# Kernel tuning notes

Hardware: AMD Instinct MI355X
Metric: run time of the kernel (lower is better)

## Reference

```python
import jax, jax.numpy as jnp
import numpy as np

B, S, E, H = 2, 2048, 1024, 16
D = E // H  # head dim = 64
ROPE_BASE = 10000.0


def _rope(x):
    # x: [B, H, S, D]; interleaved-pair rotary embeddings (torchtune style)
    d2 = D // 2
    theta = 1.0 / (ROPE_BASE ** (jnp.arange(d2, dtype=jnp.float32) * 2.0 / D))  # [D/2]
    pos = jnp.arange(S, dtype=jnp.float32)
    ang = pos[:, None] * theta[None, :]            # [S, D/2]
    cos, sin = jnp.cos(ang), jnp.sin(ang)          # broadcast over B,H
    xr = x.reshape(B, H, S, d2, 2)
    x1, x2 = xr[..., 0], xr[..., 1]
    o1 = x1 * cos - x2 * sin
    o2 = x1 * sin + x2 * cos
    return jnp.stack([o1, o2], axis=-1).reshape(B, H, S, D)


def setup_inputs() -> dict:
    key = jax.random.key(0)
    ks = jax.random.split(key, 5)
    scale = 1.0 / np.sqrt(E)
    return {
        "x": jax.random.normal(ks[0], (B, S, E), dtype=jnp.float32),
        "Wq": jax.random.normal(ks[1], (E, E), dtype=jnp.float32) * scale,
        "Wk": jax.random.normal(ks[2], (E, E), dtype=jnp.float32) * scale,
        "Wv": jax.random.normal(ks[3], (E, E), dtype=jnp.float32) * scale,
        "Wo": jax.random.normal(ks[4], (E, E), dtype=jnp.float32) * scale,
    }


def reference(x, Wq, Wk, Wv, Wo):
    # torch Linear: y = x @ W^T
    def proj(W):
        return (x @ W.T).reshape(B, S, H, D).transpose(0, 2, 1, 3)  # [B,H,S,D]

    q = _rope(proj(Wq))
    k = _rope(proj(Wk))
    v = proj(Wv)

    attn_scale = 1.0 / np.sqrt(E)  # faithful: scales by sqrt(d_embed), not head dim
    scores = jnp.einsum('bhqd,bhkd->bhqk', q, k) * attn_scale  # [B,H,S,S]
    causal = jnp.tril(jnp.ones((S, S), dtype=bool))
    scores = jnp.where(causal, scores, -jnp.inf)
    probs = jax.nn.softmax(scores, axis=-1)
    out = jnp.einsum('bhqk,bhkd->bhqd', probs, v)  # [B,H,S,D]
    out = out.transpose(0, 2, 1, 3).reshape(B, S, E)
    return out @ Wo.T
```

## Files before the change

kernel.cpp:

```cpp
#include <hip/hip_runtime.h>
#include <hip/hip_bf16.h>
#include <math.h>

typedef __bf16 bf16;
typedef __bf16 bf16x8 __attribute__((ext_vector_type(8)));
typedef float f32x4 __attribute__((ext_vector_type(4)));

#define SEQ 2048
#define EMB 1024
#define NH  16
#define HD  64
#define NROWS 4096

#define GLOAD_LDS16(gp, lp)                                             \
    __builtin_amdgcn_global_load_lds(                                   \
        (const __attribute__((address_space(1))) void*)(gp),            \
        (__attribute__((address_space(3))) void*)(lp), 16, 0, 0)

__global__ __launch_bounds__(256) void cvt_kernel(
    const float* __restrict__ x,  const float* __restrict__ Wq,
    const float* __restrict__ Wk, const float* __restrict__ Wv,
    const float* __restrict__ Wo,
    bf16* __restrict__ xb, bf16* __restrict__ Wqb, bf16* __restrict__ Wkb,
    bf16* __restrict__ Wvb, bf16* __restrict__ Wob)
{
    int b = blockIdx.x;
    const float* src; bf16* dst; int boff;
    if      (b < 2048) { src = x;  dst = xb;  boff = b;        }
    else if (b < 2560) { src = Wq; dst = Wqb; boff = b - 2048; }
    else if (b < 3072) { src = Wk; dst = Wkb; boff = b - 2560; }
    else if (b < 3584) { src = Wv; dst = Wvb; boff = b - 3072; }
    else               { src = Wo; dst = Wob; boff = b - 3584; }
    size_t off = (size_t)boff * 2048 + (size_t)threadIdx.x * 8;
    float4 f0 = *(const float4*)(src + off);
    float4 f1 = *(const float4*)(src + off + 4);
    bf16x8 v;
    v[0] = (bf16)f0.x; v[1] = (bf16)f0.y; v[2] = (bf16)f0.z; v[3] = (bf16)f0.w;
    v[4] = (bf16)f1.x; v[5] = (bf16)f1.y; v[6] = (bf16)f1.z; v[7] = (bf16)f1.w;
    *(bf16x8*)(dst + off) = v;
}

__global__ void rope_table_kernel(float* __restrict__ ctab, float* __restrict__ stab) {
    int t = blockIdx.x * blockDim.x + threadIdx.x;
    int s = t >> 5;
    int j = t & 31;
    double freq = pow(10000.0, -(double)j / 32.0);
    double ang = (double)s * freq;
    ctab[t] = (float)cos(ang);
    stab[t] = (float)sin(ang);
}

__global__ __launch_bounds__(256) void qkv_rope_kernel(
    const bf16* __restrict__ x,
    const bf16* __restrict__ Wq, const bf16* __restrict__ Wk, const bf16* __restrict__ Wv,
    const float* __restrict__ ctab, const float* __restrict__ stab,
    bf16* __restrict__ q_ws, bf16* __restrict__ kf_ws, bf16* __restrict__ vf_ws)
{
    __shared__ __align__(16) bf16 As[128 * 32];
    __shared__ __align__(16) bf16 Bs[128 * 32];

    const int t    = threadIdx.x;
    const int lane = t & 63;
    const int wave = t >> 6;
    const int col  = lane & 15;
    const int quad = lane >> 4;

    const int nblk = blockIdx.x;
    const int m0   = blockIdx.y * 128;

    const bf16* W; int nloc;
    if (nblk < 8)       { W = Wq; nloc = nblk * 128; }
    else if (nblk < 16) { W = Wk; nloc = (nblk - 8) * 128; }
    else                { W = Wv; nloc = (nblk - 16) * 128; }

    const bf16 *ga[2], *gb[2];
#pragma unroll
    for (int j = 0; j < 2; j++) {
        int c = t + j * 256;
        ga[j] = x + (size_t)(m0 + (c >> 2)) * EMB + (c & 3) * 8;
        gb[j] = W + (size_t)(nloc + (c >> 2)) * EMB + (c & 3) * 8;
    }

    const int wm = (wave >> 1) * 64;
    const int wn = (wave & 1) * 64;

    f32x4 acc[4][4];
#pragma unroll
    for (int i = 0; i < 4; i++)
#pragma unroll
        for (int j = 0; j < 4; j++) acc[i][j] = (f32x4){0.f, 0.f, 0.f, 0.f};

    for (int kc = 0; kc < EMB; kc += 32) {
#pragma unroll
        for (int j = 0; j < 2; j++) {
            int c = t + j * 256;
            GLOAD_LDS16(ga[j] + kc, As + c * 8);
            GLOAD_LDS16(gb[j] + kc, Bs + c * 8);
        }
        __syncthreads();
        bf16x8 a[4], b[4];
#pragma unroll
        for (int mt = 0; mt < 4; mt++)
            a[mt] = *(const bf16x8*)(As + (wm + mt * 16 + col) * 32 + quad * 8);
#pragma unroll
        for (int nt = 0; nt < 4; nt++)
            b[nt] = *(const bf16x8*)(Bs + (wn + nt * 16 + col) * 32 + quad * 8);
#pragma unroll
        for (int mt = 0; mt < 4; mt++)
#pragma unroll
            for (int nt = 0; nt < 4; nt++)
                acc[mt][nt] = __builtin_amdgcn_mfma_f32_16x16x32_bf16(a[mt], b[nt], acc[mt][nt], 0, 0, 0);
        __syncthreads();
    }

    const int n0w = nblk * 128 + wn;
    const int m0w = m0 + wm;
#pragma unroll
    for (int mt = 0; mt < 4; mt++) {
#pragma unroll
        for (int nt = 0; nt < 4; nt++) {
            int n  = n0w + nt * 16 + col;
            int d  = n & 63;
            int h  = (n >> 6) & 15;
            int jj = d >> 1;
#pragma unroll
            for (int r = 0; r < 4; r++) {
                int m  = m0w + mt * 16 + quad * 4 + r;
                int bb_ = m >> 11;
                int ss = m & (SEQ - 1);
                int bh = bb_ * NH + h;
                float v = acc[mt][nt][r];
                if (n < 2048) {
                    float partner = __shfl_xor(v, 1, 64);
                    float c  = ctab[ss * 32 + jj];
                    float sn = stab[ss * 32 + jj];
                    float o = ((d & 1) == 0) ? (v * c - partner * sn)
                                             : (partner * sn + v * c);
                    if (n < 1024) {
                        q_ws[((size_t)bh * SEQ + ss) * HD + d] = (bf16)(o * 0.03125f);
                    } else {
                        size_t idx = ((size_t)(bh * 128 + (ss >> 4)) * 2 + (d >> 5)) * 512
                                   + ((d >> 3) & 3) * 128 + (ss & 15) * 8 + (d & 7);
                        kf_ws[idx] = (bf16)o;
                    }
                } else {
                    size_t idx = ((size_t)(bh * 64 + (ss >> 5)) * 4 + ((d >> 4) & 3)) * 512
                               + ((ss >> 3) & 3) * 128 + (d & 15) * 8 + (ss & 7);
                    vf_ws[idx] = (bf16)v;
                }
            }
        }
    }
}

__global__ __launch_bounds__(128) void attn_kernel(
    const bf16* __restrict__ q_ws, const bf16* __restrict__ kf,
    const bf16* __restrict__ vf, bf16* __restrict__ attn_ws)
{
    __shared__ float comb_o[2][4][4][64];
    __shared__ float comb_l[2][64];

    const int lane = threadIdx.x & 63;
    const int wave = threadIdx.x >> 6;
    const int col  = lane & 15;
    const int quad = lane >> 4;

    const int qt = 63 - (int)(blockIdx.x >> 5);
    const int bh = blockIdx.x & 31;
    const int b_ = bh >> 4;
    const int h  = bh & 15;
    const int qb = qt * 32;
    const int nk = qt + 1;

    const bf16* Q  = q_ws + (size_t)bh * SEQ * HD;
    const bf16* Kf = kf + (size_t)bh * 131072;
    const bf16* Vf = vf + (size_t)bh * 131072;

    bf16x8 aq[2][2];
#pragma unroll
    for (int f = 0; f < 2; f++) {
        const bf16* qp = Q + (size_t)(qb + f * 16 + col) * HD + quad * 8;
        aq[f][0] = *(const bf16x8*)(qp);
        aq[f][1] = *(const bf16x8*)(qp + 32);
    }

    f32x4 acc_o[2][4];
#pragma unroll
    for (int f = 0; f < 2; f++)
#pragma unroll
        for (int i = 0; i < 4; i++) acc_o[f][i] = (f32x4){0.f, 0.f, 0.f, 0.f};
    float lsum[2] = {0.f, 0.f};

    int psrc[8];
#pragma unroll
    for (int j = 0; j < 8; j++)
        psrc[j] = ((((quad * 2 + (j >> 2)) & 3) << 4) | col) << 2;

    int s0 = (wave < nk) ? wave : 0;
    bf16x8 Ka[2][2], nKa[2][2];
    {
        const bf16* p = Kf + (size_t)s0 * 2048 + lane * 8;
        Ka[0][0] = *(const bf16x8*)(p);
        Ka[0][1] = *(const bf16x8*)(p + 512);
        Ka[1][0] = *(const bf16x8*)(p + 1024);
        Ka[1][1] = *(const bf16x8*)(p + 1536);
    }

    for (int s = wave; s < nk; s += 2) {
        bf16x8 Vb[4];
        {
            const bf16* p = Vf + (size_t)s * 2048 + lane * 8;
            Vb[0] = *(const bf16x8*)(p);
            Vb[1] = *(const bf16x8*)(p + 512);
            Vb[2] = *(const bf16x8*)(p + 1024);
            Vb[3] = *(const bf16x8*)(p + 1536);
        }

        f32x4 sT[2][2];
#pragma unroll
        for (int g = 0; g < 2; g++)
#pragma unroll
            for (int f = 0; f < 2; f++) {
                f32x4 z = (f32x4){0.f, 0.f, 0.f, 0.f};
                z = __builtin_amdgcn_mfma_f32_16x16x32_bf16(Ka[g][0], aq[f][0], z, 0, 0, 0);
                z = __builtin_amdgcn_mfma_f32_16x16x32_bf16(Ka[g][1], aq[f][1], z, 0, 0, 0);
                sT[g][f] = z;
            }

        {
            int sn = (s + 2 < nk) ? s + 2 : s;
            const bf16* p = Kf + (size_t)sn * 2048 + lane * 8;
            nKa[0][0] = *(const bf16x8*)(p);
            nKa[0][1] = *(const bf16x8*)(p + 512);
            nKa[1][0] = *(const bf16x8*)(p + 1024);
            nKa[1][1] = *(const bf16x8*)(p + 1536);
        }

        float p[2][2][4];
        if (s == nk - 1) {
#pragma unroll
            for (int g = 0; g < 2; g++)
#pragma unroll
                for (int f = 0; f < 2; f++) {
                    const int qg = qb + f * 16 + col;
#pragma unroll
                    for (int r = 0; r < 4; r++) {
                        int key = s * 32 + g * 16 + quad * 4 + r;
                        float e = (key <= qg) ? __expf(sT[g][f][r]) : 0.f;
                        p[g][f][r] = e;
                        lsum[f] += e;
                    }
                }
        } else {
#pragma unroll
            for (int g = 0; g < 2; g++)
#pragma unroll
                for (int f = 0; f < 2; f++)
#pragma unroll
                    for (int r = 0; r < 4; r++) {
                        float e = __expf(sT[g][f][r]);
                        p[g][f][r] = e;
                        lsum[f] += e;
                    }
        }

#pragma unroll
        for (int f = 0; f < 2; f++) {
            unsigned int pk[4];
#pragma unroll
            for (int r = 0; r < 4; r++) {
                unsigned int lo = __builtin_bit_cast(unsigned short, (bf16)p[0][f][r]);
                unsigned int hi = __builtin_bit_cast(unsigned short, (bf16)p[1][f][r]);
                pk[r] = (hi << 16) | lo;
            }
            bf16x8 a_p;
#pragma unroll
            for (int j = 0; j < 8; j++) {
                unsigned int g = (unsigned int)__builtin_amdgcn_ds_bpermute(psrc[j], (int)pk[j & 3]);
                unsigned short bits = (quad < 2) ? (unsigned short)(g & 0xffff)
                                                 : (unsigned short)(g >> 16);
                a_p[j] = __builtin_bit_cast(bf16, bits);
            }
#pragma unroll
            for (int nt = 0; nt < 4; nt++)
                acc_o[f][nt] = __builtin_amdgcn_mfma_f32_16x16x32_bf16(a_p, Vb[nt], acc_o[f][nt], 0, 0, 0);
        }

        Ka[0][0] = nKa[0][0]; Ka[0][1] = nKa[0][1];
        Ka[1][0] = nKa[1][0]; Ka[1][1] = nKa[1][1];
    }

    if (wave == 1) {
#pragma unroll
        for (int f = 0; f < 2; f++) {
            comb_l[f][lane] = lsum[f];
#pragma unroll
            for (int nt = 0; nt < 4; nt++)
#pragma unroll
                for (int r = 0; r < 4; r++)
                    comb_o[f][nt][r][lane] = acc_o[f][nt][r];
        }
    }
    __syncthreads();

    if (wave == 0) {
#pragma unroll
        for (int f = 0; f < 2; f++) {
            lsum[f] += comb_l[f][lane];
#pragma unroll
            for (int nt = 0; nt < 4; nt++)
#pragma unroll
                for (int r = 0; r < 4; r++)
                    acc_o[f][nt][r] += comb_o[f][nt][r][lane];
        }

#pragma unroll
        for (int f = 0; f < 2; f++) {
            lsum[f] += __shfl_xor(lsum[f], 16, 64);
            lsum[f] += __shfl_xor(lsum[f], 32, 64);
        }
#pragma unroll
        for (int f = 0; f < 2; f++)
#pragma unroll
            for (int r = 0; r < 4; r++) {
                float l_r = __shfl(lsum[f], quad * 4 + r, 64);
                float inv = 1.0f / l_r;
                int q = qb + f * 16 + quad * 4 + r;
                bf16* orow = attn_ws + (size_t)(b_ * SEQ + q) * EMB + h * HD;
#pragma unroll
                for (int nt = 0; nt < 4; nt++)
                    orow[nt * 16 + col] = (bf16)(acc_o[f][nt][r] * inv);
            }
    }
}

__global__ __launch_bounds__(256) void oproj_kernel(
    const bf16* __restrict__ attn_ws, const bf16* __restrict__ Wo,
    float* __restrict__ out)
{
    __shared__ __align__(16) bf16 As[128 * 32];
    __shared__ __align__(16) bf16 Bs[64 * 32];

    const int t    = threadIdx.x;
    const int lane = t & 63;
    const int wave = t >> 6;
    const int col  = lane & 15;
    const int quad = lane >> 4;

    const int n0 = blockIdx.x * 64;
    const int m0 = blockIdx.y * 128;

    const bf16 *ga[2], *gb;
#pragma unroll
    for (int j = 0; j < 2; j++) {
        int c = t + j * 256;
        ga[j] = attn_ws + (size_t)(m0 + (c >> 2)) * EMB + (c & 3) * 8;
    }
    gb = Wo + (size_t)(n0 + (t >> 2)) * EMB + (t & 3) * 8;

    const int wm = (wave >> 1) * 64;
    const int wn = (wave & 1) * 32;

    f32x4 acc[4][2];
#pragma unroll
    for (int i = 0; i < 4; i++)
#pragma unroll
        for (int j = 0; j < 2; j++) acc[i][j] = (f32x4){0.f, 0.f, 0.f, 0.f};

    for (int kc = 0; kc < EMB; kc += 32) {
#pragma unroll
        for (int j = 0; j < 2; j++) {
            int c = t + j * 256;
            GLOAD_LDS16(ga[j] + kc, As + c * 8);
        }
        GLOAD_LDS16(gb + kc, Bs + t * 8);
        __syncthreads();
        bf16x8 a[4], b[2];
#pragma unroll
        for (int mt = 0; mt < 4; mt++)
            a[mt] = *(const bf16x8*)(As + (wm + mt * 16 + col) * 32 + quad * 8);
#pragma unroll
        for (int nt = 0; nt < 2; nt++)
            b[nt] = *(const bf16x8*)(Bs + (wn + nt * 16 + col) * 32 + quad * 8);
#pragma unroll
        for (int mt = 0; mt < 4; mt++)
#pragma unroll
            for (int nt = 0; nt < 2; nt++)
                acc[mt][nt] = __builtin_amdgcn_mfma_f32_16x16x32_bf16(a[mt], b[nt], acc[mt][nt], 0, 0, 0);
        __syncthreads();
    }

#pragma unroll
    for (int mt = 0; mt < 4; mt++)
#pragma unroll
        for (int nt = 0; nt < 2; nt++)
#pragma unroll
            for (int r = 0; r < 4; r++) {
                int m = m0 + wm + mt * 16 + quad * 4 + r;
                int n = n0 + wn + nt * 16 + col;
                out[(size_t)m * EMB + n] = acc[mt][nt][r];
            }
}

extern "C" void kernel_launch(void* const* d_in, const int* in_sizes, int n_in,
                              void* d_out, int out_size, void* d_ws, size_t ws_size,
                              hipStream_t stream) {
    const float* x  = (const float*)d_in[0];
    const float* Wq = (const float*)d_in[1];
    const float* Wk = (const float*)d_in[2];
    const float* Wv = (const float*)d_in[3];
    const float* Wo = (const float*)d_in[4];
    float* out = (float*)d_out;

    char* ws = (char*)d_ws;
    bf16* q_ws    = (bf16*)(ws);
    bf16* kf_ws   = (bf16*)(ws + (8u  << 20));
    bf16* vf_ws   = (bf16*)(ws + (16u << 20));
    bf16* xb      = (bf16*)(ws + (24u << 20));
    bf16* attn_ws = (bf16*)(ws + (24u << 20));
    bf16* Wqb     = (bf16*)(ws + (32u << 20));
    bf16* Wkb     = (bf16*)(ws + (34u << 20));
    bf16* Wvb     = (bf16*)(ws + (36u << 20));
    bf16* Wob     = (bf16*)(ws + (38u << 20));
    float* ctab   = (float*)(ws + (40u << 20));
    float* stab   = ctab + SEQ * 32;

    hipLaunchKernelGGL(cvt_kernel, dim3(4096), dim3(256), 0, stream,
                       x, Wq, Wk, Wv, Wo, xb, Wqb, Wkb, Wvb, Wob);
    hipLaunchKernelGGL(rope_table_kernel, dim3(SEQ * 32 / 256), dim3(256), 0, stream,
                       ctab, stab);
    hipLaunchKernelGGL(qkv_rope_kernel, dim3(24, 32), dim3(256), 0, stream,
                       xb, Wqb, Wkb, Wvb, ctab, stab, q_ws, kf_ws, vf_ws);
    hipLaunchKernelGGL(attn_kernel, dim3(2048), dim3(128), 0, stream,
                       q_ws, kf_ws, vf_ws, attn_ws);
    hipLaunchKernelGGL(oproj_kernel, dim3(16, 32), dim3(256), 0, stream,
                       attn_ws, Wob, out);
}
```

Before: 212.0 us.

## Stage GEMM epilogues through LDS for coalesced stores and fuse rope table into cvt

The QKV projection epilogue now writes each wave's results into a per-wave LDS tile, laid out in the final q, k-fragment or v-fragment order, then copies it out with 16-byte vector stores. The output projection does the same with a padded float tile and float4 stores. This replaces scattered 2- and 4-byte global stores. The rope-table computation moves into the conversion kernel as extra blocks, removing one launch. The cost is larger shared memory per block (36 KB), which may lower occupancy.

```diff
diff --git a/kernel.cpp b/kernel.cpp
--- a/kernel.cpp
+++ b/kernel.cpp
@@ -17,14 +17,25 @@
         (const __attribute__((address_space(1))) void*)(gp),            \
         (__attribute__((address_space(3))) void*)(lp), 16, 0, 0)
 
-__global__ __launch_bounds__(256) void cvt_kernel(
+__global__ __launch_bounds__(256) void cvt_rope_kernel(
     const float* __restrict__ x,  const float* __restrict__ Wq,
     const float* __restrict__ Wk, const float* __restrict__ Wv,
     const float* __restrict__ Wo,
     bf16* __restrict__ xb, bf16* __restrict__ Wqb, bf16* __restrict__ Wkb,
-    bf16* __restrict__ Wvb, bf16* __restrict__ Wob)
+    bf16* __restrict__ Wvb, bf16* __restrict__ Wob,
+    float* __restrict__ ctab, float* __restrict__ stab)
 {
     int b = blockIdx.x;
+    if (b >= 4096) {
+        int t = (b - 4096) * 256 + threadIdx.x;
+        int s = t >> 5;
+        int j = t & 31;
+        double freq = pow(10000.0, -(double)j / 32.0);
+        double ang = (double)s * freq;
+        ctab[t] = (float)cos(ang);
+        stab[t] = (float)sin(ang);
+        return;
+    }
     const float* src; bf16* dst; int boff;
     if      (b < 2048) { src = x;  dst = xb;  boff = b;        }
     else if (b < 2560) { src = Wq; dst = Wqb; boff = b - 2048; }
@@ -40,24 +51,15 @@
     *(bf16x8*)(dst + off) = v;
 }
 
-__global__ void rope_table_kernel(float* __restrict__ ctab, float* __restrict__ stab) {
-    int t = blockIdx.x * blockDim.x + threadIdx.x;
-    int s = t >> 5;
-    int j = t & 31;
-    double freq = pow(10000.0, -(double)j / 32.0);
-    double ang = (double)s * freq;
-    ctab[t] = (float)cos(ang);
-    stab[t] = (float)sin(ang);
-}
-
 __global__ __launch_bounds__(256) void qkv_rope_kernel(
     const bf16* __restrict__ x,
     const bf16* __restrict__ Wq, const bf16* __restrict__ Wk, const bf16* __restrict__ Wv,
     const float* __restrict__ ctab, const float* __restrict__ stab,
     bf16* __restrict__ q_ws, bf16* __restrict__ kf_ws, bf16* __restrict__ vf_ws)
 {
-    __shared__ __align__(16) bf16 As[128 * 32];
-    __shared__ __align__(16) bf16 Bs[128 * 32];
+    __shared__ __align__(16) bf16 SMEM[18432];
+    bf16* As = SMEM;
+    bf16* Bs = SMEM + 4096;
 
     const int t    = threadIdx.x;
     const int lane = t & 63;
@@ -113,42 +115,69 @@
         __syncthreads();
     }
 
-    const int n0w = nblk * 128 + wn;
-    const int m0w = m0 + wm;
+    bf16* Es = SMEM + wave * 4608;
+
+    const int n0w  = nblk * 128 + wn;
+    const int m0w  = m0 + wm;
+    const int bb_  = m0w >> 11;
+    const int ss0  = m0w & (SEQ - 1);
+    const int h    = (n0w >> 6) & 15;
+    const int bh   = bb_ * NH + h;
+    const int kind = (n0w < 1024) ? 0 : (n0w < 2048 ? 1 : 2);
+
 #pragma unroll
     for (int mt = 0; mt < 4; mt++) {
 #pragma unroll
         for (int nt = 0; nt < 4; nt++) {
-            int n  = n0w + nt * 16 + col;
-            int d  = n & 63;
-            int h  = (n >> 6) & 15;
-            int jj = d >> 1;
+            const int d  = nt * 16 + col;
+            const int jj = d >> 1;
 #pragma unroll
             for (int r = 0; r < 4; r++) {
-                int m  = m0w + mt * 16 + quad * 4 + r;
-                int bb_ = m >> 11;
-                int ss = m & (SEQ - 1);
-                int bh = bb_ * NH + h;
+                const int ss_l = mt * 16 + quad * 4 + r;
                 float v = acc[mt][nt][r];
-                if (n < 2048) {
+                if (kind < 2) {
                     float partner = __shfl_xor(v, 1, 64);
-                    float c  = ctab[ss * 32 + jj];
-                    float sn = stab[ss * 32 + jj];
+                    float c  = ctab[(ss0 + ss_l) * 32 + jj];
+                    float sn = stab[(ss0 + ss_l) * 32 + jj];
                     float o = ((d & 1) == 0) ? (v * c - partner * sn)
                                              : (partner * sn + v * c);
-                    if (n < 1024) {
-                        q_ws[((size_t)bh * SEQ + ss) * HD + d] = (bf16)(o * 0.03125f);
+                    if (kind == 0) {
+                        Es[ss_l * 72 + d] = (bf16)(o * 0.03125f);
                     } else {
-                        size_t idx = ((size_t)(bh * 128 + (ss >> 4)) * 2 + (d >> 5)) * 512
-                                   + ((d >> 3) & 3) * 128 + (ss & 15) * 8 + (d & 7);
-                        kf_ws[idx] = (bf16)o;
+                        int eoff = ((ss_l >> 4) * 2 + (d >> 5)) * 512
+                                 + ((d >> 3) & 3) * 128 + (ss_l & 15) * 8 + (d & 7);
+                        Es[eoff] = (bf16)o;
                     }
                 } else {
-                    size_t idx = ((size_t)(bh * 64 + (ss >> 5)) * 4 + ((d >> 4) & 3)) * 512
-                               + ((ss >> 3) & 3) * 128 + (d & 15) * 8 + (ss & 7);
-                    vf_ws[idx] = (bf16)v;
+                    int eoff = ((ss_l >> 5) * 4 + (d >> 4)) * 512
+                             + ((ss_l >> 3) & 3) * 128 + (d & 15) * 8 + (ss_l & 7);
+                    Es[eoff] = (bf16)v;
                 }
             }
+        }
+    }
+
+    const int row = lane >> 3, c8 = lane & 7;
+    if (kind == 0) {
+        bf16* qbase = q_ws + ((size_t)bh * SEQ + ss0) * HD;
+#pragma unroll
+        for (int i = 0; i < 8; i++) {
+            bf16x8 vv = *(const bf16x8*)&Es[(i * 8 + row) * 72 + c8 * 8];
+            *(bf16x8*)(qbase + (size_t)(i * 8 + row) * HD + c8 * 8) = vv;
+        }
+    } else if (kind == 1) {
+        bf16* kbase = kf_ws + ((size_t)bh * 128 + (ss0 >> 4)) * 1024;
+#pragma unroll
+        for (int i = 0; i < 8; i++) {
+            bf16x8 vv = *(const bf16x8*)&Es[i * 512 + lane * 8];
+            *(bf16x8*)(kbase + i * 512 + lane * 8) = vv;
+        }
+    } else {
+        bf16* vbase = vf_ws + ((size_t)bh * 64 + (ss0 >> 5)) * 2048;
+#pragma unroll
+        for (int i = 0; i < 8; i++) {
+            bf16x8 vv = *(const bf16x8*)&Es[i * 512 + lane * 8];
+            *(bf16x8*)(vbase + i * 512 + lane * 8) = vv;
         }
     }
 }
@@ -338,8 +367,9 @@
     const bf16* __restrict__ attn_ws, const bf16* __restrict__ Wo,
     float* __restrict__ out)
 {
-    __shared__ __align__(16) bf16 As[128 * 32];
-    __shared__ __align__(16) bf16 Bs[64 * 32];
+    __shared__ __align__(16) char SM[36864];
+    bf16* As = (bf16*)SM;
+    bf16* Bs = (bf16*)(SM + 8192);
 
     const int t    = threadIdx.x;
     const int lane = t & 63;
@@ -390,16 +420,22 @@
         __syncthreads();
     }
 
+    float* Os = (float*)(SM + (size_t)wave * 9216);
 #pragma unroll
     for (int mt = 0; mt < 4; mt++)
 #pragma unroll
         for (int nt = 0; nt < 2; nt++)
 #pragma unroll
-            for (int r = 0; r < 4; r++) {
-                int m = m0 + wm + mt * 16 + quad * 4 + r;
-                int n = n0 + wn + nt * 16 + col;
-                out[(size_t)m * EMB + n] = acc[mt][nt][r];
-            }
+            for (int r = 0; r < 4; r++)
+                Os[(mt * 16 + quad * 4 + r) * 36 + nt * 16 + col] = acc[mt][nt][r];
+
+    const int row = lane >> 3, c8 = lane & 7;
+    float* obase = out + (size_t)(m0 + wm) * EMB + n0 + wn;
+#pragma unroll
+    for (int i = 0; i < 8; i++) {
+        float4 vv = *(const float4*)&Os[(i * 8 + row) * 36 + c8 * 4];
+        *(float4*)(obase + (size_t)(i * 8 + row) * EMB + c8 * 4) = vv;
+    }
 }
 
 extern "C" void kernel_launch(void* const* d_in, const int* in_sizes, int n_in,
@@ -425,10 +461,8 @@
     float* ctab   = (float*)(ws + (40u << 20));
     float* stab   = ctab + SEQ * 32;
 
-    hipLaunchKernelGGL(cvt_kernel, dim3(4096), dim3(256), 0, stream,
-                       x, Wq, Wk, Wv, Wo, xb, Wqb, Wkb, Wvb, Wob);
-    hipLaunchKernelGGL(rope_table_kernel, dim3(SEQ * 32 / 256), dim3(256), 0, stream,
-                       ctab, stab);
+    hipLaunchKernelGGL(cvt_rope_kernel, dim3(4352), dim3(256), 0, stream,
+                       x, Wq, Wk, Wv, Wo, xb, Wqb, Wkb, Wvb, Wob, ctab, stab);
     hipLaunchKernelGGL(qkv_rope_kernel, dim3(24, 32), dim3(256), 0, stream,
                        xb, Wqb, Wkb, Wvb, ctab, stab, q_ws, kf_ws, vf_ws);
     hipLaunchKernelGGL(attn_kernel, dim3(2048), dim3(128), 0, stream,
```

New measurement: 180.7 us. 14.8% less time.
